# Kernel optimization log

Hardware: AMD Instinct MI355X
Metric: run time of the kernel (lower is better)

## Reference

```python
import jax, jax.numpy as jnp
import numpy as np

HEADS = 8
DIM = 512
DIM_HEAD = 64          # dim // 8
LANDMARKS = 256        # dim // 2
PINV_ITERS = 6
KERNEL = 33            # residual_conv_kernel
SCALE = DIM_HEAD ** -0.5
LN_EPS = 1e-5


def _moore_penrose_pinv(x, iters):
    # x: [B,H,m,m]; global (over all batches/heads) max of row/col abs sums, as in torch impl
    abs_x = jnp.abs(x)
    col = abs_x.sum(-1).max()
    row = abs_x.sum(-2).max()
    z = jnp.swapaxes(x, -1, -2) / (col * row)
    I = jnp.eye(x.shape[-1], dtype=x.dtype)
    for _ in range(iters):
        xz = x @ z
        z = 0.25 * z @ (13.0 * I - (xz @ (15.0 * I - (xz @ (7.0 * I - xz)))))
    return z


def setup_inputs() -> dict:
    key = jax.random.key(0)
    ks = jax.random.split(key, 5)
    B, N = 4, 8192
    x = jax.random.normal(ks[0], (B, N, DIM), dtype=jnp.float32)
    ln_g = jnp.ones((DIM,), jnp.float32)
    ln_b = jnp.zeros((DIM,), jnp.float32)
    w_qkv = jax.random.normal(ks[1], (DIM, 3 * HEADS * DIM_HEAD), jnp.float32) * 0.02
    w_out = jax.random.normal(ks[2], (HEADS * DIM_HEAD, DIM), jnp.float32) * 0.02
    b_out = jnp.zeros((DIM,), jnp.float32)
    res_kernel = jax.random.normal(ks[3], (HEADS, 1, KERNEL, 1), jnp.float32) * 0.02  # OIHW depthwise
    return {"x": x, "ln_g": ln_g, "ln_b": ln_b, "w_qkv": w_qkv,
            "w_out": w_out, "b_out": b_out, "res_kernel": res_kernel}


def reference(x, ln_g, ln_b, w_qkv, w_out, b_out, res_kernel):
    B, N, D = x.shape
    # pre-norm LayerNorm
    mu = x.mean(-1, keepdims=True)
    var = jnp.mean((x - mu) ** 2, axis=-1, keepdims=True)
    xn = (x - mu) * jax.lax.rsqrt(var + LN_EPS) * ln_g + ln_b
    # left-pad sequence so it divides into LANDMARKS groups (torch pads at front)
    m = LANDMARKS
    pad = (m - N % m) % m
    xp = jnp.pad(xn, ((0, 0), (pad, 0), (0, 0)))
    Np = N + pad
    qkv = xp @ w_qkv                                    # [B,Np,3*H*dh]
    q, k, v = jnp.split(qkv, 3, axis=-1)
    split_heads = lambda t: t.reshape(B, Np, HEADS, DIM_HEAD).transpose(0, 2, 1, 3)
    q, k, v = split_heads(q), split_heads(k), split_heads(v)  # [B,H,Np,dh]
    q = q * SCALE
    l = Np // m                                         # landmark group size
    q_l = q.reshape(B, HEADS, m, l, DIM_HEAD).sum(3) / l  # [B,H,m,dh]
    k_l = k.reshape(B, HEADS, m, l, DIM_HEAD).sum(3) / l
    sim1 = jnp.einsum('bhid,bhjd->bhij', q, k_l)        # [B,H,Np,m]
    sim2 = jnp.einsum('bhid,bhjd->bhij', q_l, k_l)      # [B,H,m,m]
    sim3 = jnp.einsum('bhid,bhjd->bhij', q_l, k)        # [B,H,m,Np]
    attn1 = jax.nn.softmax(sim1, axis=-1)
    attn2 = jax.nn.softmax(sim2, axis=-1)
    attn3 = jax.nn.softmax(sim3, axis=-1)
    attn2_inv = _moore_penrose_pinv(attn2, PINV_ITERS)
    out = (attn1 @ attn2_inv) @ (attn3 @ v)             # [B,H,Np,dh]
    # depthwise conv residual over sequence dim (Conv2d kernel (33,1), groups=heads)
    res = jax.lax.conv_general_dilated(
        v, res_kernel, window_strides=(1, 1),
        padding=[(KERNEL // 2, KERNEL // 2), (0, 0)],
        dimension_numbers=('NCHW', 'OIHW', 'NCHW'),
        feature_group_count=HEADS)
    out = out + res
    out = out.transpose(0, 2, 1, 3).reshape(B, Np, HEADS * DIM_HEAD)
    out = out @ w_out + b_out                           # dropout = identity (eval)
    out = out[:, -N:]                                   # drop front padding
    return x + out
```

## Files before the change

kernel.cpp:

```cpp
#include <hip/hip_runtime.h>
#include <hip/hip_bf16.h>
#include <stdint.h>

#define B_ 4
#define H_ 8
#define N_ 8192
#define D_ 512
#define M_ 256
#define BH 32
#define TOK 32768
#define SCALE 0.125f
#define LN_EPS 1e-5f

using bf16x8 = __attribute__((ext_vector_type(8))) short;
using f32x4  = __attribute__((ext_vector_type(4))) float;
typedef unsigned short u16;
typedef unsigned int   u32;

__device__ __forceinline__ float bf2f(u16 h){ union{u32 u; float f;} x; x.u = ((u32)h)<<16; return x.f; }
__device__ __forceinline__ u16 f2bf(float f){ union{float f; u32 u;} x; x.f=f; u32 r = (x.u + 0x7fffu + ((x.u>>16)&1u))>>16; return (u16)r; }
__device__ __forceinline__ f32x4 mfma16(bf16x8 a, bf16x8 b, f32x4 c){
  return __builtin_amdgcn_mfma_f32_16x16x32_bf16(a, b, c, 0, 0, 0);
}
__device__ __forceinline__ void stage16(const u16* g, u16* lds){
  __builtin_amdgcn_global_load_lds((const __attribute__((address_space(1))) unsigned int*)g,
                                   (__attribute__((address_space(3))) unsigned int*)lds, 16, 0, 0);
}

__global__ __launch_bounds__(256) void k_prep(const float* __restrict__ wqkv, const float* __restrict__ wout,
                                              u16* __restrict__ wqkvt, u16* __restrict__ woutt){
  int id = blockIdx.x*256 + threadIdx.x;
  for (int i = id; i < 1536*512; i += gridDim.x*256){ int c = i>>9, kk = i&511; wqkvt[i] = f2bf(wqkv[(size_t)kk*1536 + c]); }
  for (int i = id; i < 512*512;  i += gridDim.x*256){ int c = i>>9, kk = i&511; woutt[i] = f2bf(wout[(size_t)kk*512 + c]); }
}

__global__ __launch_bounds__(256) void k_ln(const float* __restrict__ x, const float* __restrict__ g,
                                            const float* __restrict__ bb, u16* __restrict__ xn){
  int row = blockIdx.x; int tid = threadIdx.x;
  const float* xr = x + (size_t)row*D_;
  float2 v = reinterpret_cast<const float2*>(xr)[tid];
  float s1 = v.x + v.y, s2 = v.x*v.x + v.y*v.y;
  for (int o=1;o<64;o<<=1){ s1 += __shfl_xor(s1,o); s2 += __shfl_xor(s2,o); }
  __shared__ float a1[4], a2[4];
  if ((tid&63)==0){ a1[tid>>6]=s1; a2[tid>>6]=s2; }
  __syncthreads();
  s1 = a1[0]+a1[1]+a1[2]+a1[3]; s2 = a2[0]+a2[1]+a2[2]+a2[3];
  float mu = s1*(1.f/D_);
  float var = s2*(1.f/D_) - mu*mu;
  float rs = rsqrtf(var + LN_EPS);
  float2 gg = reinterpret_cast<const float2*>(g)[tid];
  float2 b2 = reinterpret_cast<const float2*>(bb)[tid];
  u16 o0 = f2bf((v.x-mu)*rs*gg.x + b2.x);
  u16 o1 = f2bf((v.y-mu)*rs*gg.y + b2.y);
  reinterpret_cast<u32*>(xn + (size_t)row*D_)[tid] = (u32)o0 | ((u32)o1<<16);
}

__global__ __launch_bounds__(256) void k_qkv(const u16* __restrict__ A, const u16* __restrict__ Bt,
    u16* __restrict__ q, u16* __restrict__ k, u16* __restrict__ vt){
  __shared__ __align__(16) u16 As[128*32];
  __shared__ __align__(16) u16 Bs[128*32];
  int m0 = blockIdx.x*128, n0 = blockIdx.y*128;
  int tid = threadIdx.x, lane = tid&63, wave = tid>>6;
  int wm = wave>>1, wn = wave&1;
  int lr = lane>>2, lc = (lane&3)*8;
  f32x4 acc[4][4];
  #pragma unroll
  for (int i=0;i<4;i++)
    #pragma unroll
    for (int j=0;j<4;j++) acc[i][j] = (f32x4)0.f;
  for (int k0=0;k0<512;k0+=32){
    #pragma unroll
    for (int i=0;i<2;i++){
      int c = wave + i*4;
      stage16(&A [(size_t)(m0 + c*16 + lr)*512 + k0 + lc], &As[c*16*32]);
      stage16(&Bt[(size_t)(n0 + c*16 + lr)*512 + k0 + lc], &Bs[c*16*32]);
    }
    asm volatile("s_waitcnt vmcnt(0)" ::: "memory");
    __syncthreads();
    bf16x8 a[4], b[4];
    #pragma unroll
    for (int mi=0;mi<4;mi++) a[mi] = *reinterpret_cast<const bf16x8*>(&As[(wm*64+mi*16+(lane&15))*32 + (lane>>4)*8]);
    #pragma unroll
    for (int ni=0;ni<4;ni++) b[ni] = *reinterpret_cast<const bf16x8*>(&Bs[(wn*64+ni*16+(lane&15))*32 + (lane>>4)*8]);
    #pragma unroll
    for (int mi=0;mi<4;mi++)
      #pragma unroll
      for (int ni=0;ni<4;ni++)
        acc[mi][ni] = mfma16(a[mi], b[ni], acc[mi][ni]);
    __syncthreads();
  }
  #pragma unroll
  for (int mi=0;mi<4;mi++){
    int gr0 = m0 + wm*64 + mi*16 + ((lane>>4)<<2);
    #pragma unroll
    for (int ni=0;ni<4;ni++){
      int gc = n0 + wn*64 + ni*16 + (lane&15);
      int t = gc>>9, wi = gc&511, h = wi>>6, d = wi&63;
      #pragma unroll
      for (int r=0;r<4;r++){
        int row = gr0 + r; int bq = row>>13, n = row & (N_-1);
        float val = acc[mi][ni][r];
        size_t bhh = (size_t)(bq*H_+h);
        if (t==0)      q[(bhh*N_ + n)*64 + d] = f2bf(val*SCALE);
        else if (t==1) k[(bhh*N_ + n)*64 + d] = f2bf(val);
        else           vt[(bhh*64 + d)*N_ + n] = f2bf(val);
      }
    }
  }
}

__global__ __launch_bounds__(64) void k_land(const u16* __restrict__ q, const u16* __restrict__ k,
                                             u16* __restrict__ ql, u16* __restrict__ kl){
  int bh = blockIdx.x >> 8, j = blockIdx.x & 255, d = threadIdx.x;
  size_t base = ((size_t)bh*N_ + j*32)*64 + d;
  float sq=0.f, sk=0.f;
  #pragma unroll
  for (int i=0;i<32;i++){ sq += bf2f(q[base + (size_t)i*64]); sk += bf2f(k[base + (size_t)i*64]); }
  size_t o = ((size_t)bh*256 + j)*64 + d;
  ql[o] = f2bf(sq*(1.f/32.f)); kl[o] = f2bf(sk*(1.f/32.f));
}

__global__ __launch_bounds__(256) void k_attn2(const u16* __restrict__ ql, const u16* __restrict__ kl,
                                               float* __restrict__ X, float* __restrict__ Xt){
  int bh = blockIdx.x >> 8, i = blockIdx.x & 255, j = threadIdx.x;
  __shared__ float qrow[64];
  __shared__ float red[256];
  if (j < 64) qrow[j] = bf2f(ql[((size_t)bh*256+i)*64 + j]);
  __syncthreads();
  const u16* kr = kl + ((size_t)bh*256 + j)*64;
  float s = 0.f;
  #pragma unroll
  for (int d=0; d<64; d++) s += qrow[d]*bf2f(kr[d]);
  red[j] = s; __syncthreads();
  for (int o=128;o>0;o>>=1){ if (j<o) red[j] = fmaxf(red[j], red[j+o]); __syncthreads(); }
  float mx = red[0]; __syncthreads();
  float e = __expf(s - mx);
  red[j] = e; __syncthreads();
  for (int o=128;o>0;o>>=1){ if (j<o) red[j] += red[j+o]; __syncthreads(); }
  float p = e / red[0];
  X [((size_t)bh*256+i)*256 + j] = p;
  Xt[((size_t)bh*256+j)*256 + i] = p;
}

__global__ __launch_bounds__(256) void k_pinvstats(const float* __restrict__ X, float* __restrict__ sc){
  int bh = blockIdx.x, t = threadIdx.x;
  const float* Xb = X + ((size_t)bh<<16);
  float cs=0.f, rs=0.f;
  for (int i=0;i<256;i++) cs += Xb[(size_t)i*256 + t];
  for (int j=0;j<256;j++) rs += Xb[(size_t)t*256 + j];
  __shared__ float r1[256], r2[256];
  r1[t]=cs; r2[t]=rs; __syncthreads();
  for (int o=128;o>0;o>>=1){ if (t<o){ r1[t]=fmaxf(r1[t],r1[t+o]); r2[t]=fmaxf(r2[t],r2[t+o]); } __syncthreads(); }
  if (t==0) sc[bh] = 1.f/(r1[0]*r2[0]);
}

__global__ __launch_bounds__(256) void k_pinvinit(const float* __restrict__ X, const float* __restrict__ Xt,
     const float* __restrict__ sc, u16* Xhi, u16* Xlo, u16* Znhi, u16* Znlo, u16* Zthi, u16* Ztlo){
  size_t i = (size_t)blockIdx.x*256 + threadIdx.x;
  int bh = (int)(i>>16);
  float s = sc[bh];
  float xv = X[i];  u16 h1 = f2bf(xv);  Xhi[i]=h1;  Xlo[i]=f2bf(xv - bf2f(h1));
  float zn = Xt[i]*s; u16 h2 = f2bf(zn); Znhi[i]=h2; Znlo[i]=f2bf(zn - bf2f(h2));
  float zt = xv*s;  u16 h3 = f2bf(zt);  Zthi[i]=h3; Ztlo[i]=f2bf(zt - bf2f(h3));
}

template<int MODE>
__global__ __launch_bounds__(256) void k_mmhl(
    const u16* Ahi, const u16* Alo,
    const u16* Bthi, const u16* Btlo,
    u16* Chi, u16* Clo,
    const u16* Znhi, const u16* Znlo,
    const u16* B1hi, const u16* B1lo,
    const u16* B2hi, const u16* B2lo,
    u16* Zothi, u16* Zotlo)
{
  __shared__ __align__(16) u16 AhS[64*32];
  __shared__ __align__(16) u16 AlS[64*32];
  __shared__ __align__(16) u16 BhS[64*32];
  __shared__ __align__(16) u16 BlS[64*32];
  int bh = blockIdx.z;
  int m0 = blockIdx.x*64, n0 = blockIdx.y*64;
  size_t base = ((size_t)bh)<<16;
  int tid = threadIdx.x, lane = tid&63, wave = tid>>6;
  int wm = wave>>1, wn = wave&1;
  int lr = lane>>2, lc = (lane&3)*8;
  f32x4 acc[2][2];
  #pragma unroll
  for (int i=0;i<2;i++)
    #pragma unroll
    for (int j=0;j<2;j++) acc[i][j] = (f32x4)0.f;
  for (int k0=0;k0<256;k0+=32){
    stage16(&Ahi [base + (size_t)(m0 + wave*16 + lr)*256 + k0 + lc], &AhS[wave*16*32]);
    stage16(&Alo [base + (size_t)(m0 + wave*16 + lr)*256 + k0 + lc], &AlS[wave*16*32]);
    stage16(&Bthi[base + (size_t)(n0 + wave*16 + lr)*256 + k0 + lc], &BhS[wave*16*32]);
    stage16(&Btlo[base + (size_t)(n0 + wave*16 + lr)*256 + k0 + lc], &BlS[wave*16*32]);
    asm volatile("s_waitcnt vmcnt(0)" ::: "memory");
    __syncthreads();
    bf16x8 ah[2], al2[2], bh2[2], bl2[2];
    #pragma unroll
    for (int mi=0;mi<2;mi++){
      int rr = wm*32 + mi*16 + (lane&15);
      ah[mi]  = *reinterpret_cast<const bf16x8*>(&AhS[rr*32 + (lane>>4)*8]);
      al2[mi] = *reinterpret_cast<const bf16x8*>(&AlS[rr*32 + (lane>>4)*8]);
    }
    #pragma unroll
    for (int ni=0;ni<2;ni++){
      int rr = wn*32 + ni*16 + (lane&15);
      bh2[ni] = *reinterpret_cast<const bf16x8*>(&BhS[rr*32 + (lane>>4)*8]);
      bl2[ni] = *reinterpret_cast<const bf16x8*>(&BlS[rr*32 + (lane>>4)*8]);
    }
    #pragma unroll
    for (int mi=0;mi<2;mi++)
      #pragma unroll
      for (int ni=0;ni<2;ni++){
        f32x4 c = acc[mi][ni];
        c = mfma16(ah[mi],  bh2[ni], c);
        c = mfma16(ah[mi],  bl2[ni], c);
        c = mfma16(al2[mi], bh2[ni], c);
        acc[mi][ni] = c;
      }
    __syncthreads();
  }
  #pragma unroll
  for (int mi=0;mi<2;mi++){
    #pragma unroll
    for (int ni=0;ni<2;ni++){
      int gr0 = m0 + wm*32 + mi*16 + ((lane>>4)<<2);
      int gc  = n0 + wn*32 + ni*16 + (lane&15);
      #pragma unroll
      for (int rr=0;rr<4;rr++){
        int gr = gr0 + rr;
        float val = acc[mi][ni][rr];
        if (MODE==0){
          size_t o = base + (size_t)gr*256 + gc;
          u16 hh = f2bf(val); Chi[o]=hh; Clo[o]=f2bf(val - bf2f(hh));
        } else if (MODE==1){
          size_t o = base + (size_t)gc*256 + gr;
          u16 hh = f2bf(val); Chi[o]=hh; Clo[o]=f2bf(val - bf2f(hh));
        } else {
          size_t o = base + (size_t)gr*256 + gc;
          float z  = bf2f(Znhi[o]) + bf2f(Znlo[o]);
          float b1 = bf2f(B1hi[o]) + bf2f(B1lo[o]);
          float b2 = bf2f(B2hi[o]) + bf2f(B2lo[o]);
          float zn = 0.25f*(13.f*z - 15.f*b1 + 7.f*b2 - val);
          u16 hh = f2bf(zn); u16 ll = f2bf(zn - bf2f(hh));
          Chi[o] = hh; Clo[o] = ll;
          size_t ot = base + (size_t)gc*256 + gr;
          Zothi[ot] = hh; Zotlo[ot] = ll;
        }
      }
    }
  }
}

__global__ __launch_bounds__(256) void k_flashw(const u16* __restrict__ ql, const u16* __restrict__ kb,
                                                const u16* __restrict__ vt,
                                                float* __restrict__ part, float* __restrict__ lpart){
  __shared__ __align__(16) u16 P[4][64][40];
  int kc = blockIdx.x, bh = blockIdx.y;
  int tid = threadIdx.x, lane = tid&63, wave = tid>>6;
  bf16x8 aq[4][2];
  #pragma unroll
  for (int mi=0;mi<4;mi++){
    int row = wave*64 + mi*16 + (lane&15);
    #pragma unroll
    for (int ks=0;ks<2;ks++)
      aq[mi][ks] = *reinterpret_cast<const bf16x8*>(&ql[((size_t)bh*256 + row)*64 + ks*32 + (lane>>4)*8]);
  }
  f32x4 acc[4][4];
  float rs[4][4];
  #pragma unroll
  for (int i=0;i<4;i++)
    #pragma unroll
    for (int j=0;j<4;j++){ acc[i][j] = (f32x4)0.f; rs[i][j] = 0.f; }
  for (int step=0; step<16; step++){
    int nb = kc*512 + step*32;
    f32x4 s[4][2];
    #pragma unroll
    for (int ci=0;ci<2;ci++){
      int j = nb + ci*16 + (lane&15);
      const u16* kr = &kb[((size_t)bh*N_ + j)*64 + (lane>>4)*8];
      bf16x8 b0 = *reinterpret_cast<const bf16x8*>(kr);
      bf16x8 b1 = *reinterpret_cast<const bf16x8*>(kr + 32);
      #pragma unroll
      for (int mi=0;mi<4;mi++)
        s[mi][ci] = mfma16(aq[mi][1], b1, mfma16(aq[mi][0], b0, (f32x4)0.f));
    }
    #pragma unroll
    for (int mi=0;mi<4;mi++)
      #pragma unroll
      for (int ci=0;ci<2;ci++)
        #pragma unroll
        for (int rr=0;rr<4;rr++){
          float e = __expf(s[mi][ci][rr]);
          rs[mi][rr] += e;
          P[wave][mi*16 + ((lane>>4)<<2) + rr][ci*16 + (lane&15)] = f2bf(e);
        }
    __syncthreads();
    bf16x8 ap[4];
    #pragma unroll
    for (int mi=0;mi<4;mi++)
      ap[mi] = *reinterpret_cast<const bf16x8*>(&P[wave][mi*16 + (lane&15)][(lane>>4)*8]);
    #pragma unroll
    for (int ci=0;ci<4;ci++){
      int d = ci*16 + (lane&15);
      bf16x8 bv = *reinterpret_cast<const bf16x8*>(&vt[((size_t)bh*64 + d)*N_ + nb + (lane>>4)*8]);
      #pragma unroll
      for (int mi=0;mi<4;mi++)
        acc[mi][ci] = mfma16(ap[mi], bv, acc[mi][ci]);
    }
    __syncthreads();
  }
  #pragma unroll
  for (int mi=0;mi<4;mi++)
    #pragma unroll
    for (int rr=0;rr<4;rr++){
      float v2 = rs[mi][rr];
      v2 += __shfl_xor(v2,1); v2 += __shfl_xor(v2,2); v2 += __shfl_xor(v2,4); v2 += __shfl_xor(v2,8);
      rs[mi][rr] = v2;
    }
  size_t pb = ((size_t)kc*32 + bh)*256;
  #pragma unroll
  for (int mi=0;mi<4;mi++){
    int r0 = wave*64 + mi*16 + ((lane>>4)<<2);
    #pragma unroll
    for (int ci=0;ci<4;ci++){
      int d = ci*16 + (lane&15);
      #pragma unroll
      for (int rr=0;rr<4;rr++)
        part[(pb + r0 + rr)*64 + d] = acc[mi][ci][rr];
    }
    if ((lane&15)==0){
      #pragma unroll
      for (int rr=0;rr<4;rr++)
        lpart[pb + r0 + rr] = rs[mi][rr];
    }
  }
}

__global__ __launch_bounds__(256) void k_wfin(const float* __restrict__ part, const float* __restrict__ lpart,
                                              float* __restrict__ w){
  int idx = blockIdx.x*256 + threadIdx.x;
  int bh = idx>>14, within = idx & 16383, r = within>>6;
  float s = 0.f, l = 0.f;
  #pragma unroll
  for (int c=0;c<16;c++){
    s += part [(size_t)(c*32+bh)*16384 + within];
    l += lpart[(size_t)(c*32+bh)*256 + r];
  }
  w[idx] = s / l;
}

__global__ __launch_bounds__(64) void k_w2(const u16* __restrict__ Zhi, const u16* __restrict__ Zlo,
                                           const float* __restrict__ w, u16* __restrict__ w2t){
  int bh = blockIdx.x>>8, j = blockIdx.x&255, d = threadIdx.x;
  size_t zb = ((size_t)bh<<16) + (size_t)j*256;
  float acc = 0.f;
  for (int i=0;i<256;i++){
    float zv = bf2f(Zhi[zb+i]) + bf2f(Zlo[zb+i]);
    acc += zv * w[((size_t)bh*256 + i)*64 + d];
  }
  w2t[((size_t)bh*64 + d)*256 + j] = f2bf(acc);
}

__global__ __launch_bounds__(256) void k_conv(const u16* __restrict__ vt, const float* __restrict__ kern,
                                              u16* __restrict__ res_t){
  int t = threadIdx.x;
  int d = blockIdx.y, bh = blockIdx.z;
  int n0 = blockIdx.x*2048 + t*8;
  const u16* src = vt + ((size_t)bh*64 + d)*N_;
  const float* kh = kern + (bh&7)*33;
  float xv[40];
  #pragma unroll
  for (int vv=0; vv<5; vv++){
    int nb = n0 - 16 + vv*8;
    if (nb >= 0 && nb + 8 <= N_) {
      bf16x8 raw = *reinterpret_cast<const bf16x8*>(src + nb);
      #pragma unroll
      for (int j=0;j<8;j++) xv[vv*8+j] = bf2f((u16)raw[j]);
    } else {
      #pragma unroll
      for (int j=0;j<8;j++){
        int n = nb + j;
        xv[vv*8+j] = (n>=0 && n<N_) ? bf2f(src[n]) : 0.f;
      }
    }
  }
  float c[33];
  #pragma unroll
  for (int kk2=0;kk2<33;kk2++) c[kk2] = kh[kk2];
  u16 outv[8];
  #pragma unroll
  for (int j=0;j<8;j++){
    float acc = 0.f;
    #pragma unroll
    for (int kk2=0;kk2<33;kk2++) acc += xv[j+kk2]*c[kk2];
    outv[j] = f2bf(acc);
  }
  *reinterpret_cast<bf16x8*>(res_t + ((size_t)bh*64 + d)*N_ + n0) = *reinterpret_cast<bf16x8*>(outv);
}

__global__ __launch_bounds__(256) void k_attn1(const u16* __restrict__ q, const u16* __restrict__ kl,
   const u16* __restrict__ w2t, const u16* __restrict__ res_t, u16* __restrict__ cc)
{
  __shared__ __align__(16) u16 P[4][32][136];
  int n0 = blockIdx.x*128, bh = blockIdx.y;
  int tid = threadIdx.x, lane = tid&63, wave = tid>>6;
  int bq = bh>>3, h = bh&7;
  bf16x8 a[2][2];
  #pragma unroll
  for (int mi=0;mi<2;mi++){
    int n = n0 + wave*32 + mi*16 + (lane&15);
    #pragma unroll
    for (int ks=0;ks<2;ks++)
      a[mi][ks] = *reinterpret_cast<const bf16x8*>(&q[((size_t)bh*N_ + n)*64 + ks*32 + (lane>>4)*8]);
  }
  float rowsum[2][4];
  #pragma unroll
  for (int mi=0;mi<2;mi++)
    #pragma unroll
    for (int rr=0;rr<4;rr++) rowsum[mi][rr]=0.f;
  f32x4 acco[2][4];
  #pragma unroll
  for (int mi=0;mi<2;mi++)
    #pragma unroll
    for (int ci=0;ci<4;ci++) acco[mi][ci] = (f32x4)0.f;

  #pragma unroll
  for (int half=0; half<2; half++){
    f32x4 accs[2][8];
    #pragma unroll
    for (int mi=0;mi<2;mi++)
      #pragma unroll
      for (int ci=0;ci<8;ci++) accs[mi][ci] = (f32x4)0.f;
    #pragma unroll
    for (int ci=0;ci<8;ci++){
      int j = (half*8+ci)*16 + (lane&15);
      bf16x8 b0 = *reinterpret_cast<const bf16x8*>(&kl[((size_t)bh*256 + j)*64 + (lane>>4)*8]);
      bf16x8 b1 = *reinterpret_cast<const bf16x8*>(&kl[((size_t)bh*256 + j)*64 + 32 + (lane>>4)*8]);
      #pragma unroll
      for (int mi=0;mi<2;mi++){
        f32x4 c = accs[mi][ci];
        c = mfma16(a[mi][0], b0, c);
        c = mfma16(a[mi][1], b1, c);
        accs[mi][ci] = c;
      }
    }
    #pragma unroll
    for (int mi=0;mi<2;mi++)
      #pragma unroll
      for (int ci=0;ci<8;ci++)
        #pragma unroll
        for (int rr=0;rr<4;rr++){
          float e = __expf(accs[mi][ci][rr]);
          rowsum[mi][rr] += e;
          P[wave][mi*16 + ((lane>>4)<<2) + rr][ci*16 + (lane&15)] = f2bf(e);
        }
    __syncthreads();
    #pragma unroll
    for (int ks=0;ks<4;ks++){
      bf16x8 a2[2];
      #pragma unroll
      for (int mi=0;mi<2;mi++)
        a2[mi] = *reinterpret_cast<const bf16x8*>(&P[wave][mi*16 + (lane&15)][ks*32 + (lane>>4)*8]);
      #pragma unroll
      for (int ci=0;ci<4;ci++){
        bf16x8 b2 = *reinterpret_cast<const bf16x8*>(&w2t[((size_t)bh*64 + ci*16 + (lane&15))*256 + half*128 + ks*32 + (lane>>4)*8]);
        #pragma unroll
        for (int mi=0;mi<2;mi++)
          acco[mi][ci] = mfma16(a2[mi], b2, acco[mi][ci]);
      }
    }
    __syncthreads();
  }
  #pragma unroll
  for (int mi=0;mi<2;mi++)
    #pragma unroll
    for (int rr=0;rr<4;rr++){
      float s = rowsum[mi][rr];
      s += __shfl_xor(s,1); s += __shfl_xor(s,2); s += __shfl_xor(s,4); s += __shfl_xor(s,8);
      rowsum[mi][rr] = s;
    }
  #pragma unroll
  for (int mi=0;mi<2;mi++){
    int nb = n0 + wave*32 + mi*16 + ((lane>>4)<<2);
    #pragma unroll
    for (int ci=0;ci<4;ci++){
      int d = ci*16 + (lane&15);
      #pragma unroll
      for (int rr=0;rr<4;rr++){
        int n = nb + rr;
        float val = acco[mi][ci][rr] / rowsum[mi][rr];
        val += bf2f(res_t[((size_t)bh*64 + d)*N_ + n]);
        cc[((size_t)bq*N_ + n)*512 + h*64 + d] = f2bf(val);
      }
    }
  }
}

__global__ __launch_bounds__(256) void k_out(const u16* __restrict__ A, const u16* __restrict__ Bt,
     const float* __restrict__ bo, const float* __restrict__ x, float* __restrict__ out){
  __shared__ __align__(16) u16 As[128*32];
  __shared__ __align__(16) u16 Bs[128*32];
  int m0 = blockIdx.x*128, n0 = blockIdx.y*128;
  int tid = threadIdx.x, lane = tid&63, wave = tid>>6;
  int wm = wave>>1, wn = wave&1;
  int lr = lane>>2, lc = (lane&3)*8;
  f32x4 acc[4][4];
  #pragma unroll
  for (int i=0;i<4;i++)
    #pragma unroll
    for (int j=0;j<4;j++) acc[i][j] = (f32x4)0.f;
  for (int k0=0;k0<512;k0+=32){
    #pragma unroll
    for (int i=0;i<2;i++){
      int c = wave + i*4;
      stage16(&A [(size_t)(m0 + c*16 + lr)*512 + k0 + lc], &As[c*16*32]);
      stage16(&Bt[(size_t)(n0 + c*16 + lr)*512 + k0 + lc], &Bs[c*16*32]);
    }
    asm volatile("s_waitcnt vmcnt(0)" ::: "memory");
    __syncthreads();
    bf16x8 a[4], b[4];
    #pragma unroll
    for (int mi=0;mi<4;mi++) a[mi] = *reinterpret_cast<const bf16x8*>(&As[(wm*64+mi*16+(lane&15))*32 + (lane>>4)*8]);
    #pragma unroll
    for (int ni=0;ni<4;ni++) b[ni] = *reinterpret_cast<const bf16x8*>(&Bs[(wn*64+ni*16+(lane&15))*32 + (lane>>4)*8]);
    #pragma unroll
    for (int mi=0;mi<4;mi++)
      #pragma unroll
      for (int ni=0;ni<4;ni++)
        acc[mi][ni] = mfma16(a[mi], b[ni], acc[mi][ni]);
    __syncthreads();
  }
  #pragma unroll
  for (int mi=0;mi<4;mi++){
    int gr0 = m0 + wm*64 + mi*16 + ((lane>>4)<<2);
    #pragma unroll
    for (int ni=0;ni<4;ni++){
      int gc = n0 + wn*64 + ni*16 + (lane&15);
      float bv = bo[gc];
      #pragma unroll
      for (int r=0;r<4;r++){
        int row = gr0 + r;
        out[(size_t)row*512 + gc] = acc[mi][ni][r] + bv + x[(size_t)row*512 + gc];
      }
    }
  }
}

extern "C" void kernel_launch(void* const* d_in, const int* in_sizes, int n_in,
                              void* d_out, int out_size, void* d_ws, size_t ws_size,
                              hipStream_t stream) {
  (void)in_sizes; (void)n_in; (void)out_size;
  const float* x     = (const float*)d_in[0];
  const float* ln_g  = (const float*)d_in[1];
  const float* ln_b  = (const float*)d_in[2];
  const float* w_qkv = (const float*)d_in[3];
  const float* w_out = (const float*)d_in[4];
  const float* b_out = (const float*)d_in[5];
  const float* res_k = (const float*)d_in[6];
  float* out = (float*)d_out;

  char* ws = (char*)d_ws;
  size_t off = 0;
  auto alloc = [&](size_t n)->char*{ char* r = ws + off; off += (n + 255) & ~(size_t)255; return r; };

  u16* xn     = (u16*)alloc((size_t)TOK*512*2);
  u16* cc     = xn;
  u16* wqkvt  = (u16*)alloc(1536*512*2);
  u16* woutt  = (u16*)alloc(512*512*2);
  u16* qb     = (u16*)alloc((size_t)BH*N_*64*2);
  u16* kb     = (u16*)alloc((size_t)BH*N_*64*2);
  u16* vt     = (u16*)alloc((size_t)BH*N_*64*2);
  u16* ql     = (u16*)alloc((size_t)BH*256*64*2);
  u16* kl     = (u16*)alloc((size_t)BH*256*64*2);
  float* X    = (float*)alloc((size_t)BH*65536*4);
  float* Xt   = (float*)alloc((size_t)BH*65536*4);
  float* sc   = (float*)alloc(32*4);
  u16* Xhi    = (u16*)alloc((size_t)BH*65536*2);
  u16* Xlo    = (u16*)alloc((size_t)BH*65536*2);
  u16* Znh    = (u16*)alloc((size_t)BH*65536*2);
  u16* Znl    = (u16*)alloc((size_t)BH*65536*2);
  u16* Zth    = (u16*)alloc((size_t)BH*65536*2);
  u16* Ztl    = (u16*)alloc((size_t)BH*65536*2);
  u16* B2h    = (u16*)alloc((size_t)BH*65536*2);
  u16* B2l    = (u16*)alloc((size_t)BH*65536*2);
  u16* res_t  = (u16*)alloc((size_t)BH*64*N_*2);
  size_t need = off;
  if (ws_size < need) return;

  u16* A1th = (u16*)X;
  u16* A1tl = (u16*)X + (size_t)BH*65536;
  u16* B1h  = (u16*)Xt;
  u16* B1l  = (u16*)Xt + (size_t)BH*65536;

  char* ob = (char*)d_out;
  float* part  = (float*)(ob);
  float* lpart = (float*)(ob + 33554432);
  float* wbuf  = (float*)(ob + 34078720);
  u16*   w2t   = (u16*)  (ob + 36175872);

  k_prep<<<dim3(512),256,0,stream>>>(w_qkv, w_out, wqkvt, woutt);
  k_ln<<<dim3(TOK),256,0,stream>>>(x, ln_g, ln_b, xn);
  k_qkv<<<dim3(256,12),256,0,stream>>>(xn, wqkvt, qb, kb, vt);
  k_land<<<dim3(8192),64,0,stream>>>(qb, kb, ql, kl);
  k_attn2<<<dim3(8192),256,0,stream>>>(ql, kl, X, Xt);
  k_pinvstats<<<dim3(32),256,0,stream>>>(X, sc);
  k_pinvinit<<<dim3(8192),256,0,stream>>>(X, Xt, sc, Xhi, Xlo, Znh, Znl, Zth, Ztl);

  dim3 gmm(4,4,32);
  for (int it=0; it<6; it++){
    k_mmhl<1><<<gmm,256,0,stream>>>(Xhi,Xlo, Zth,Ztl, A1th,A1tl,
        nullptr,nullptr,nullptr,nullptr,nullptr,nullptr, nullptr,nullptr);
    k_mmhl<0><<<gmm,256,0,stream>>>(Znh,Znl, A1th,A1tl, B1h,B1l,
        nullptr,nullptr,nullptr,nullptr,nullptr,nullptr, nullptr,nullptr);
    k_mmhl<0><<<gmm,256,0,stream>>>(B1h,B1l, A1th,A1tl, B2h,B2l,
        nullptr,nullptr,nullptr,nullptr,nullptr,nullptr, nullptr,nullptr);
    k_mmhl<2><<<gmm,256,0,stream>>>(B2h,B2l, A1th,A1tl, Znh,Znl,
        Znh,Znl, B1h,B1l, B2h,B2l, Zth,Ztl);
  }

  k_flashw<<<dim3(16,32),256,0,stream>>>(ql, kb, vt, part, lpart);
  k_wfin<<<dim3(2048),256,0,stream>>>(part, lpart, wbuf);
  k_w2<<<dim3(8192),64,0,stream>>>(Znh, Znl, wbuf, w2t);
  k_conv<<<dim3(4,64,32),256,0,stream>>>(vt, res_k, res_t);
  k_attn1<<<dim3(64,32),256,0,stream>>>(qb, kl, w2t, res_t, cc);
  k_out<<<dim3(256,4),256,0,stream>>>(cc, woutt, b_out, x, out);
}
```

Baseline: 1.002 ms.

## Double-buffer LDS tiles in QKV, pinv, and output GEMM kernels

Adds ping-pong shared-memory buffers to three GEMM kernels so the next K-tile's global-to-LDS load is issued before computing on the current tile, with a partial vmcnt wait. This is meant to hide global load latency behind MFMA work. It doubles LDS usage per block, which may lower occupancy. The vmcnt(4) count relies on the number of loads issued per stage16 call.

```diff
diff --git a/kernel.cpp b/kernel.cpp
--- a/kernel.cpp
+++ b/kernel.cpp
@@ -57,8 +57,8 @@
 
 __global__ __launch_bounds__(256) void k_qkv(const u16* __restrict__ A, const u16* __restrict__ Bt,
     u16* __restrict__ q, u16* __restrict__ k, u16* __restrict__ vt){
-  __shared__ __align__(16) u16 As[128*32];
-  __shared__ __align__(16) u16 Bs[128*32];
+  __shared__ __align__(16) u16 As[2][128*32];
+  __shared__ __align__(16) u16 Bs[2][128*32];
   int m0 = blockIdx.x*128, n0 = blockIdx.y*128;
   int tid = threadIdx.x, lane = tid&63, wave = tid>>6;
   int wm = wave>>1, wn = wave&1;
@@ -68,20 +68,30 @@
   for (int i=0;i<4;i++)
     #pragma unroll
     for (int j=0;j<4;j++) acc[i][j] = (f32x4)0.f;
-  for (int k0=0;k0<512;k0+=32){
+
+  auto stage_tile = [&](int k0, int buf){
     #pragma unroll
     for (int i=0;i<2;i++){
       int c = wave + i*4;
-      stage16(&A [(size_t)(m0 + c*16 + lr)*512 + k0 + lc], &As[c*16*32]);
-      stage16(&Bt[(size_t)(n0 + c*16 + lr)*512 + k0 + lc], &Bs[c*16*32]);
-    }
-    asm volatile("s_waitcnt vmcnt(0)" ::: "memory");
+      stage16(&A [(size_t)(m0 + c*16 + lr)*512 + k0 + lc], &As[buf][c*16*32]);
+      stage16(&Bt[(size_t)(n0 + c*16 + lr)*512 + k0 + lc], &Bs[buf][c*16*32]);
+    }
+  };
+  stage_tile(0, 0);
+  for (int it=0; it<16; it++){
+    int cur = it&1;
+    if (it<15){
+      stage_tile((it+1)*32, cur^1);
+      asm volatile("s_waitcnt vmcnt(4)" ::: "memory");
+    } else {
+      asm volatile("s_waitcnt vmcnt(0)" ::: "memory");
+    }
     __syncthreads();
     bf16x8 a[4], b[4];
     #pragma unroll
-    for (int mi=0;mi<4;mi++) a[mi] = *reinterpret_cast<const bf16x8*>(&As[(wm*64+mi*16+(lane&15))*32 + (lane>>4)*8]);
-    #pragma unroll
-    for (int ni=0;ni<4;ni++) b[ni] = *reinterpret_cast<const bf16x8*>(&Bs[(wn*64+ni*16+(lane&15))*32 + (lane>>4)*8]);
+    for (int mi=0;mi<4;mi++) a[mi] = *reinterpret_cast<const bf16x8*>(&As[cur][(wm*64+mi*16+(lane&15))*32 + (lane>>4)*8]);
+    #pragma unroll
+    for (int ni=0;ni<4;ni++) b[ni] = *reinterpret_cast<const bf16x8*>(&Bs[cur][(wn*64+ni*16+(lane&15))*32 + (lane>>4)*8]);
     #pragma unroll
     for (int mi=0;mi<4;mi++)
       #pragma unroll
@@ -174,10 +184,10 @@
     const u16* B2hi, const u16* B2lo,
     u16* Zothi, u16* Zotlo)
 {
-  __shared__ __align__(16) u16 AhS[64*32];
-  __shared__ __align__(16) u16 AlS[64*32];
-  __shared__ __align__(16) u16 BhS[64*32];
-  __shared__ __align__(16) u16 BlS[64*32];
+  __shared__ __align__(16) u16 AhS[2][64*32];
+  __shared__ __align__(16) u16 AlS[2][64*32];
+  __shared__ __align__(16) u16 BhS[2][64*32];
+  __shared__ __align__(16) u16 BlS[2][64*32];
   int bh = blockIdx.z;
   int m0 = blockIdx.x*64, n0 = blockIdx.y*64;
   size_t base = ((size_t)bh)<<16;
@@ -189,25 +199,35 @@
   for (int i=0;i<2;i++)
     #pragma unroll
     for (int j=0;j<2;j++) acc[i][j] = (f32x4)0.f;
-  for (int k0=0;k0<256;k0+=32){
-    stage16(&Ahi [base + (size_t)(m0 + wave*16 + lr)*256 + k0 + lc], &AhS[wave*16*32]);
-    stage16(&Alo [base + (size_t)(m0 + wave*16 + lr)*256 + k0 + lc], &AlS[wave*16*32]);
-    stage16(&Bthi[base + (size_t)(n0 + wave*16 + lr)*256 + k0 + lc], &BhS[wave*16*32]);
-    stage16(&Btlo[base + (size_t)(n0 + wave*16 + lr)*256 + k0 + lc], &BlS[wave*16*32]);
-    asm volatile("s_waitcnt vmcnt(0)" ::: "memory");
+
+  auto stage_tile = [&](int k0, int buf){
+    stage16(&Ahi [base + (size_t)(m0 + wave*16 + lr)*256 + k0 + lc], &AhS[buf][wave*16*32]);
+    stage16(&Alo [base + (size_t)(m0 + wave*16 + lr)*256 + k0 + lc], &AlS[buf][wave*16*32]);
+    stage16(&Bthi[base + (size_t)(n0 + wave*16 + lr)*256 + k0 + lc], &BhS[buf][wave*16*32]);
+    stage16(&Btlo[base + (size_t)(n0 + wave*16 + lr)*256 + k0 + lc], &BlS[buf][wave*16*32]);
+  };
+  stage_tile(0, 0);
+  for (int it=0; it<8; it++){
+    int cur = it&1;
+    if (it<7){
+      stage_tile((it+1)*32, cur^1);
+      asm volatile("s_waitcnt vmcnt(4)" ::: "memory");
+    } else {
+      asm volatile("s_waitcnt vmcnt(0)" ::: "memory");
+    }
     __syncthreads();
     bf16x8 ah[2], al2[2], bh2[2], bl2[2];
     #pragma unroll
     for (int mi=0;mi<2;mi++){
       int rr = wm*32 + mi*16 + (lane&15);
-      ah[mi]  = *reinterpret_cast<const bf16x8*>(&AhS[rr*32 + (lane>>4)*8]);
-      al2[mi] = *reinterpret_cast<const bf16x8*>(&AlS[rr*32 + (lane>>4)*8]);
+      ah[mi]  = *reinterpret_cast<const bf16x8*>(&AhS[cur][rr*32 + (lane>>4)*8]);
+      al2[mi] = *reinterpret_cast<const bf16x8*>(&AlS[cur][rr*32 + (lane>>4)*8]);
     }
     #pragma unroll
     for (int ni=0;ni<2;ni++){
       int rr = wn*32 + ni*16 + (lane&15);
-      bh2[ni] = *reinterpret_cast<const bf16x8*>(&BhS[rr*32 + (lane>>4)*8]);
-      bl2[ni] = *reinterpret_cast<const bf16x8*>(&BlS[rr*32 + (lane>>4)*8]);
+      bh2[ni] = *reinterpret_cast<const bf16x8*>(&BhS[cur][rr*32 + (lane>>4)*8]);
+      bl2[ni] = *reinterpret_cast<const bf16x8*>(&BlS[cur][rr*32 + (lane>>4)*8]);
     }
     #pragma unroll
     for (int mi=0;mi<2;mi++)
@@ -500,8 +520,8 @@
 
 __global__ __launch_bounds__(256) void k_out(const u16* __restrict__ A, const u16* __restrict__ Bt,
      const float* __restrict__ bo, const float* __restrict__ x, float* __restrict__ out){
-  __shared__ __align__(16) u16 As[128*32];
-  __shared__ __align__(16) u16 Bs[128*32];
+  __shared__ __align__(16) u16 As[2][128*32];
+  __shared__ __align__(16) u16 Bs[2][128*32];
   int m0 = blockIdx.x*128, n0 = blockIdx.y*128;
   int tid = threadIdx.x, lane = tid&63, wave = tid>>6;
   int wm = wave>>1, wn = wave&1;
@@ -511,20 +531,30 @@
   for (int i=0;i<4;i++)
     #pragma unroll
     for (int j=0;j<4;j++) acc[i][j] = (f32x4)0.f;
-  for (int k0=0;k0<512;k0+=32){
+
+  auto stage_tile = [&](int k0, int buf){
     #pragma unroll
     for (int i=0;i<2;i++){
       int c = wave + i*4;
-      stage16(&A [(size_t)(m0 + c*16 + lr)*512 + k0 + lc], &As[c*16*32]);
-      stage16(&Bt[(size_t)(n0 + c*16 + lr)*512 + k0 + lc], &Bs[c*16*32]);
-    }
-    asm volatile("s_waitcnt vmcnt(0)" ::: "memory");
+      stage16(&A [(size_t)(m0 + c*16 + lr)*512 + k0 + lc], &As[buf][c*16*32]);
+      stage16(&Bt[(size_t)(n0 + c*16 + lr)*512 + k0 + lc], &Bs[buf][c*16*32]);
+    }
+  };
+  stage_tile(0, 0);
+  for (int it=0; it<16; it++){
+    int cur = it&1;
+    if (it<15){
+      stage_tile((it+1)*32, cur^1);
+      asm volatile("s_waitcnt vmcnt(4)" ::: "memory");
+    } else {
+      asm volatile("s_waitcnt vmcnt(0)" ::: "memory");
+    }
     __syncthreads();
     bf16x8 a[4], b[4];
     #pragma unroll
-    for (int mi=0;mi<4;mi++) a[mi] = *reinterpret_cast<const bf16x8*>(&As[(wm*64+mi*16+(lane&15))*32 + (lane>>4)*8]);
-    #pragma unroll
-    for (int ni=0;ni<4;ni++) b[ni] = *reinterpret_cast<const bf16x8*>(&Bs[(wn*64+ni*16+(lane&15))*32 + (lane>>4)*8]);
+    for (int mi=0;mi<4;mi++) a[mi] = *reinterpret_cast<const bf16x8*>(&As[cur][(wm*64+mi*16+(lane&15))*32 + (lane>>4)*8]);
+    #pragma unroll
+    for (int ni=0;ni<4;ni++) b[ni] = *reinterpret_cast<const bf16x8*>(&Bs[cur][(wn*64+ni*16+(lane&15))*32 + (lane>>4)*8]);
     #pragma unroll
     for (int mi=0;mi<4;mi++)
       #pragma unroll
```

Result: slower. 1.043 ms (+4.0%).
